# Optimization experiments

Hardware: AMD Instinct MI355X
Metric: run time of the kernel (lower is better)

## Reference

```python
import jax, jax.numpy as jnp
import numpy as np

NUM_HEADS = 16


def setup_inputs() -> dict:
    key = jax.random.key(0)
    k1, k2, k3, k4 = jax.random.split(key, 4)
    B, S, D = 4, 2048, 1024
    x = jax.random.normal(k1, (B, S, D), dtype=jnp.float32)
    mask = jnp.ones((B, S, S), dtype=jnp.int32)
    wq = jax.random.normal(k2, (D, D), dtype=jnp.float32) * (D ** -0.5)
    wk = jax.random.normal(k3, (D, D), dtype=jnp.float32) * (D ** -0.5)
    wv = jax.random.normal(k4, (D, D), dtype=jnp.float32) * (D ** -0.5)
    return {"x": x, "mask": mask, "wq": wq, "wk": wk, "wv": wv}


def reference(x, mask, wq, wk, wv):
    B, S, D = x.shape
    H = NUM_HEADS
    d_k = D // H
    # torch Linear (no bias): y = x @ W.T ; split heads -> [B,H,S,d_k]
    q = (x @ wq.T).reshape(B, S, H, d_k).transpose(0, 2, 1, 3)
    k = (x @ wk.T).reshape(B, S, H, d_k).transpose(0, 2, 1, 3)
    v = (x @ wv.T).reshape(B, S, H, d_k).transpose(0, 2, 1, 3)
    scale = 1.0 / np.sqrt(d_k).astype(np.float32)
    scores = jnp.einsum("bhqd,bhkd->bhqk", q, k) * scale  # [B,H,S,S]
    # masked_fill(mask==0, -1e9); mask broadcast over heads; NO softmax
    scores = jnp.where(mask[:, None, :, :] == 0, jnp.float32(-1e9), scores)
    # dropout is identity in eval mode
    attn = jnp.einsum("bhqk,bhkd->bhqd", scores, v)  # [B,H,S,d_k]
    return attn.transpose(0, 2, 1, 3).reshape(B, S, D)
```

## Files before the change

kernel.cpp:

```cpp
#include <hip/hip_runtime.h>


using u16 = unsigned short;
typedef __attribute__((ext_vector_type(8))) short  short8;
typedef __attribute__((ext_vector_type(4))) short  s16x4;
typedef __attribute__((ext_vector_type(4))) float  f32x4;
typedef __attribute__((ext_vector_type(4))) unsigned short u16x4;
typedef __attribute__((ext_vector_type(4))) int    i32x4;

#define DEV static __device__ __forceinline__

DEV u16 f2b(float f) {
  unsigned u = __float_as_uint(f);
  return (u16)((u + 0x7FFFu + ((u >> 16) & 1u)) >> 16);
}

DEV int swz(int row, int col) { return (row << 6) + (col ^ ((row & 7) << 3)); }

template <typename T>
DEV void gload_lds16(const T* g, T* l) {
  __builtin_amdgcn_global_load_lds((const __attribute__((address_space(1))) unsigned int*)g,
                                   (__attribute__((address_space(3))) unsigned int*)l, 16, 0, 0);
}

__global__ __launch_bounds__(256) void k_convert(const float* __restrict__ x,
                                                 const float* __restrict__ wq,
                                                 const float* __restrict__ wk,
                                                 const float* __restrict__ wv,
                                                 u16* __restrict__ xb, u16* __restrict__ wb) {
  const int NX4 = 2097152;
  const int NW4 = 262144;
  const int total = NX4 + 3 * NW4;
  for (int i = blockIdx.x * blockDim.x + threadIdx.x; i < total; i += gridDim.x * blockDim.x) {
    const float4* src; u16* dst; int j;
    if (i < NX4) { src = (const float4*)x; dst = xb; j = i; }
    else {
      int tw = i - NX4; int wsel = tw >> 18; j = tw & (NW4 - 1);
      src = (const float4*)(wsel == 0 ? wq : (wsel == 1 ? wk : wv));
      dst = wb + (size_t)wsel * 1048576;
    }
    float4 v = src[j];
    u16x4 o; o[0] = f2b(v.x); o[1] = f2b(v.y); o[2] = f2b(v.z); o[3] = f2b(v.w);
    *(u16x4*)(dst + (size_t)j * 4) = o;
  }
}

__global__ __launch_bounds__(256) void k_flags(const int* __restrict__ mask, int* __restrict__ flags) {
  const int bx = blockIdx.x;
  const int b_ = bx >> 9, rem = bx & 511, qt = rem >> 5, kt = rem & 31;
  const int t = threadIdx.x;
  const size_t base = ((size_t)(b_ * 2048 + qt * 128)) * 2048 + kt * 64;
  int az = 0;
#pragma unroll
  for (int kk = 0; kk < 8; ++kk) {
    int i = t + kk * 256;
    int row = i >> 4, c4 = i & 15;
    i32x4 v = *(const i32x4*)(mask + base + (size_t)row * 2048 + c4 * 4);
    az |= (v.x == 0) | (v.y == 0) | (v.z == 0) | (v.w == 0);
  }
  __shared__ int red[4];
  unsigned long long bal = __ballot(az != 0);
  if ((t & 63) == 0) red[t >> 6] = (bal != 0ull);
  __syncthreads();
  if (t == 0) flags[bx] = red[0] | red[1] | red[2] | red[3];
}

__global__ __launch_bounds__(256, 2) void k_proj(const u16* __restrict__ xb, const u16* __restrict__ wb,
                                                 u16* __restrict__ qb, u16* __restrict__ kb,
                                                 u16* __restrict__ vtb) {
  __shared__ u16 lA[128 * 64];
  __shared__ u16 lB[128 * 64];
  const int t = threadIdx.x, wid = t >> 6, lid = t & 63, ln = lid & 15, hi = lid >> 4;
  const int mt = blockIdx.x >> 3, nt = blockIdx.x & 7, which = blockIdx.y;
  const u16* wsrc = wb + (size_t)which * (1024 * 1024);
  const int wm = wid >> 1, wn = wid & 1;

  f32x4 acc[4][4];
#pragma unroll
  for (int a = 0; a < 4; ++a)
#pragma unroll
    for (int b2 = 0; b2 < 4; ++b2) acc[a][b2] = (f32x4){0.f, 0.f, 0.f, 0.f};

  for (int kt = 0; kt < 16; ++kt) {
    __syncthreads();
#pragma unroll
    for (int i = 0; i < 4; ++i) {
      int e = (i * 256 + t) * 8, row = e >> 6;
      int c = (e & 63) ^ ((row & 7) << 3);
      gload_lds16(xb + (size_t)(mt * 128 + row) * 1024 + kt * 64 + c, &lA[i * 2048 + wid * 512]);
      gload_lds16(wsrc + (size_t)(nt * 128 + row) * 1024 + kt * 64 + c, &lB[i * 2048 + wid * 512]);
    }
    __syncthreads();
#pragma unroll
    for (int ks = 0; ks < 2; ++ks) {
      short8 af[4], bfr[4];
#pragma unroll
      for (int mi = 0; mi < 4; ++mi) af[mi] = *(const short8*)&lA[swz(wm * 64 + mi * 16 + ln, ks * 32 + hi * 8)];
#pragma unroll
      for (int ni = 0; ni < 4; ++ni) bfr[ni] = *(const short8*)&lB[swz(wn * 64 + ni * 16 + ln, ks * 32 + hi * 8)];
#pragma unroll
      for (int mi = 0; mi < 4; ++mi)
#pragma unroll
        for (int ni = 0; ni < 4; ++ni)
          acc[mi][ni] = __builtin_amdgcn_mfma_f32_16x16x32_bf16(af[mi], bfr[ni], acc[mi][ni], 0, 0, 0);
    }
  }

  const int m0 = mt * 128 + wm * 64, n0 = nt * 128 + wn * 64;
  if (which == 2) {
#pragma unroll
    for (int mi = 0; mi < 4; ++mi)
#pragma unroll
      for (int ni = 0; ni < 4; ++ni) {
        int mm = m0 + mi * 16 + hi * 4;
        int nn = n0 + ni * 16 + ln;
        int bb = mm >> 11, s0 = mm & 2047, hh = nn >> 6, dd = nn & 63;
        u16x4 pk;
#pragma unroll
        for (int r = 0; r < 4; ++r) pk[r] = f2b(acc[mi][ni][r]);
        *(u16x4*)(vtb + ((size_t)((bb * 16 + hh) * 64 + dd)) * 2048 + s0) = pk;
      }
  } else {
    u16* dst = (which == 1) ? kb : qb;
#pragma unroll
    for (int mi = 0; mi < 4; ++mi)
#pragma unroll
      for (int ni = 0; ni < 4; ++ni) {
        int nn = n0 + ni * 16 + ln;
        int hh = nn >> 6, dd = nn & 63;
#pragma unroll
        for (int r = 0; r < 4; ++r) {
          int m = m0 + mi * 16 + hi * 4 + r;
          int bb = m >> 11, ss = m & 2047;
          dst[((size_t)(bb * 16 + hh) * 2048 + ss) * 64 + dd] = f2b(acc[mi][ni][r]);
        }
      }
  }
}

__global__ __launch_bounds__(256, 2) void k_attn(const u16* __restrict__ qb, const u16* __restrict__ kb,
                                                 const u16* __restrict__ vtb, const int* __restrict__ mask,
                                                 const int* __restrict__ flags, float* __restrict__ out) {
  __shared__ __align__(16) u16 lds[24576];
  const int t = threadIdx.x, wid = t >> 6, lid = t & 63, ln = lid & 15, hi = lid >> 4;
  const int qt = blockIdx.x, bh = blockIdx.y, b_ = bh >> 4, h = bh & 15;
  const u16* Qg = qb + (size_t)bh * (2048 * 64);
  const u16* Kg = kb + (size_t)bh * (2048 * 64);
  const u16* Vg = vtb + (size_t)bh * (64 * 2048);
  const int* flagp = flags + (b_ * 16 + qt) * 32;
  const int* maskp = mask + (size_t)b_ * (2048 * 2048);
  u16* lQ = lds + 16384;

#pragma unroll
  for (int i = 0; i < 4; ++i) {
    int e = (i * 256 + t) * 8, row = e >> 6;
    int c = (e & 63) ^ ((row & 7) << 3);
    gload_lds16(Qg + (size_t)(qt * 128 + row) * 64 + c, &lQ[i * 2048 + wid * 512]);
  }
#pragma unroll
  for (int i = 0; i < 2; ++i) {
    int e = (i * 256 + t) * 8, row = e >> 6;
    int c = (e & 63) ^ ((row & 7) << 3);
    gload_lds16(Kg + (size_t)row * 64 + c, &lds[i * 2048 + wid * 512]);
    gload_lds16(Vg + (size_t)row * 2048 + c, &lds[4096 + i * 2048 + wid * 512]);
  }
  __syncthreads();

  short8 aq[2][2];
#pragma unroll
  for (int mi = 0; mi < 2; ++mi)
#pragma unroll
    for (int ks = 0; ks < 2; ++ks)
      aq[mi][ks] = *(const short8*)&lQ[swz(wid * 32 + mi * 16 + ln, ks * 32 + hi * 8)];

  f32x4 ot[4][2];
#pragma unroll
  for (int di = 0; di < 4; ++di)
#pragma unroll
    for (int mi = 0; mi < 2; ++mi) ot[di][mi] = (f32x4){0.f, 0.f, 0.f, 0.f};

  int cur = 0;
  for (int kt = 0; kt < 32; ++kt) {
    if (kt + 1 < 32) {
#pragma unroll
      for (int i = 0; i < 2; ++i) {
        int e = (i * 256 + t) * 8, row = e >> 6;
        int c = (e & 63) ^ ((row & 7) << 3);
        gload_lds16(Kg + (size_t)((kt + 1) * 64 + row) * 64 + c, &lds[(cur ^ 1) * 8192 + i * 2048 + wid * 512]);
        gload_lds16(Vg + (size_t)row * 2048 + (kt + 1) * 64 + c, &lds[(cur ^ 1) * 8192 + 4096 + i * 2048 + wid * 512]);
      }
    }
    const u16* bK = lds + cur * 8192;
    const u16* bV = lds + cur * 8192 + 4096;

    f32x4 sa[4][2];
#pragma unroll
    for (int ni = 0; ni < 4; ++ni)
#pragma unroll
      for (int mi = 0; mi < 2; ++mi) sa[ni][mi] = (f32x4){0.f, 0.f, 0.f, 0.f};
#pragma unroll
    for (int ks = 0; ks < 2; ++ks) {
      short8 bk[4];
#pragma unroll
      for (int ni = 0; ni < 4; ++ni) bk[ni] = *(const short8*)&bK[swz(ni * 16 + ln, ks * 32 + hi * 8)];
#pragma unroll
      for (int ni = 0; ni < 4; ++ni)
#pragma unroll
        for (int mi = 0; mi < 2; ++mi)
          sa[ni][mi] = __builtin_amdgcn_mfma_f32_16x16x32_bf16(bk[ni], aq[mi][ks], sa[ni][mi], 0, 0, 0);
    }

    int flg = flagp[kt];
    s16x4 pt[4][2];
#pragma unroll
    for (int ni = 0; ni < 4; ++ni)
#pragma unroll
      for (int mi = 0; mi < 2; ++mi) {
#pragma unroll
        for (int r = 0; r < 4; ++r) {
          float p = sa[ni][mi][r] * 0.125f;
          if (flg) {
            int qg = qt * 128 + wid * 32 + mi * 16 + ln;
            int kvg = kt * 64 + ni * 16 + hi * 4 + r;
            if (maskp[(size_t)qg * 2048 + kvg] == 0) p = -1e9f;
          }
          pt[ni][mi][r] = (short)f2b(p);
        }
      }

#pragma unroll
    for (int di = 0; di < 4; ++di) {
      s16x4 vt[4];
#pragma unroll
      for (int ni = 0; ni < 4; ++ni) vt[ni] = *(const s16x4*)&bV[swz(di * 16 + ln, ni * 16 + hi * 4)];
#pragma unroll
      for (int ni = 0; ni < 4; ++ni)
#pragma unroll
        for (int mi = 0; mi < 2; ++mi)
          ot[di][mi] = __builtin_amdgcn_mfma_f32_16x16x16bf16_1k(vt[ni], pt[ni][mi], ot[di][mi], 0, 0, 0);
    }

    __syncthreads();
    cur ^= 1;
  }

  float* op = out + ((size_t)b_ * 2048 + qt * 128) * 1024 + h * 64;
#pragma unroll
  for (int di = 0; di < 4; ++di)
#pragma unroll
    for (int mi = 0; mi < 2; ++mi) {
      int q = wid * 32 + mi * 16 + ln;
      int d = di * 16 + hi * 4;
      *(f32x4*)(op + (size_t)q * 1024 + d) = ot[di][mi];
    }
}

extern "C" void kernel_launch(void* const* d_in, const int* in_sizes, int n_in,
                              void* d_out, int out_size, void* d_ws, size_t ws_size,
                              hipStream_t stream) {
  const float* x   = (const float*)d_in[0];
  const int*  mask = (const int*)d_in[1];
  const float* wq  = (const float*)d_in[2];
  const float* wk  = (const float*)d_in[3];
  const float* wv  = (const float*)d_in[4];
  float* out = (float*)d_out;

  char* ws = (char*)d_ws;
  const size_t XB_OFF = 0;
  const size_t WB_OFF = 16777216;
  const size_t QB_OFF = 23068672;
  const size_t KB_OFF = 39845888;
  const size_t VT_OFF = 56623104;
  const size_t FL_OFF = 73400320;
  if (ws_size < FL_OFF + 8192) return;

  u16* xb  = (u16*)(ws + XB_OFF);
  u16* wb  = (u16*)(ws + WB_OFF);
  u16* qb  = (u16*)(ws + QB_OFF);
  u16* kb  = (u16*)(ws + KB_OFF);
  u16* vtb = (u16*)(ws + VT_OFF);
  int* flags = (int*)(ws + FL_OFF);

  k_convert<<<2048, 256, 0, stream>>>(x, wq, wk, wv, xb, wb);
  k_flags<<<2048, 256, 0, stream>>>(mask, flags);
  k_proj<<<dim3(512, 3), 256, 0, stream>>>(xb, wb, qb, kb, vtb);
  k_attn<<<dim3(16, 64), 256, 0, stream>>>(qb, kb, vtb, mask, flags, out);
}
```

Measured before the change: 321.0 us.

## Merge prep kernels, fold Q scaling into projection, raise attention occupancy

Merges the bf16 conversion and mask-flag kernels into one launch, which removes one launch and lets both memory-bound jobs run together. Folds the 1/sqrt(d_k) scale into the Q projection epilogue so the attention loop skips a multiply per score. Loads Q fragments directly from global memory into registers instead of staging them through LDS, which shrinks LDS use enough to raise the attention launch bound to 4 blocks per CU. It also swaps the hand-written bf16 rounding for the HIP intrinsic. Rounding the pre-scaled Q to bf16 differs slightly from scaling afterwards, and the tighter launch bound may force register spills.

```diff
diff --git a/kernel.cpp b/kernel.cpp
--- a/kernel.cpp
+++ b/kernel.cpp
@@ -1,4 +1,5 @@
 #include <hip/hip_runtime.h>
+#include <hip/hip_bf16.h>
 
 
 using u16 = unsigned short;
@@ -10,9 +11,9 @@
 
 #define DEV static __device__ __forceinline__
 
-DEV u16 f2b(float f) {
-  unsigned u = __float_as_uint(f);
-  return (u16)((u + 0x7FFFu + ((u >> 16) & 1u)) >> 16);
+DEV u16 f2bh(float f) {
+  __hip_bfloat16 h = __float2bfloat16(f);
+  u16 r; __builtin_memcpy(&r, &h, 2); return r;
 }
 
 DEV int swz(int row, int col) { return (row << 6) + (col ^ ((row & 7) << 3)); }
@@ -23,46 +24,48 @@
                                    (__attribute__((address_space(3))) unsigned int*)l, 16, 0, 0);
 }
 
-__global__ __launch_bounds__(256) void k_convert(const float* __restrict__ x,
-                                                 const float* __restrict__ wq,
-                                                 const float* __restrict__ wk,
-                                                 const float* __restrict__ wv,
-                                                 u16* __restrict__ xb, u16* __restrict__ wb) {
-  const int NX4 = 2097152;
-  const int NW4 = 262144;
-  const int total = NX4 + 3 * NW4;
-  for (int i = blockIdx.x * blockDim.x + threadIdx.x; i < total; i += gridDim.x * blockDim.x) {
-    const float4* src; u16* dst; int j;
-    if (i < NX4) { src = (const float4*)x; dst = xb; j = i; }
-    else {
-      int tw = i - NX4; int wsel = tw >> 18; j = tw & (NW4 - 1);
-      src = (const float4*)(wsel == 0 ? wq : (wsel == 1 ? wk : wv));
-      dst = wb + (size_t)wsel * 1048576;
-    }
-    float4 v = src[j];
-    u16x4 o; o[0] = f2b(v.x); o[1] = f2b(v.y); o[2] = f2b(v.z); o[3] = f2b(v.w);
-    *(u16x4*)(dst + (size_t)j * 4) = o;
-  }
-}
-
-__global__ __launch_bounds__(256) void k_flags(const int* __restrict__ mask, int* __restrict__ flags) {
-  const int bx = blockIdx.x;
-  const int b_ = bx >> 9, rem = bx & 511, qt = rem >> 5, kt = rem & 31;
+__global__ __launch_bounds__(256) void k_prep(const float* __restrict__ x,
+                                              const float* __restrict__ wq,
+                                              const float* __restrict__ wk,
+                                              const float* __restrict__ wv,
+                                              const int* __restrict__ mask,
+                                              u16* __restrict__ xb, u16* __restrict__ wb,
+                                              int* __restrict__ flags) {
   const int t = threadIdx.x;
-  const size_t base = ((size_t)(b_ * 2048 + qt * 128)) * 2048 + kt * 64;
-  int az = 0;
-#pragma unroll
-  for (int kk = 0; kk < 8; ++kk) {
-    int i = t + kk * 256;
-    int row = i >> 4, c4 = i & 15;
-    i32x4 v = *(const i32x4*)(mask + base + (size_t)row * 2048 + c4 * 4);
-    az |= (v.x == 0) | (v.y == 0) | (v.z == 0) | (v.w == 0);
-  }
-  __shared__ int red[4];
-  unsigned long long bal = __ballot(az != 0);
-  if ((t & 63) == 0) red[t >> 6] = (bal != 0ull);
-  __syncthreads();
-  if (t == 0) flags[bx] = red[0] | red[1] | red[2] | red[3];
+  if (blockIdx.x < 2048) {
+    const int NX4 = 2097152;
+    const int NW4 = 262144;
+    const int total = NX4 + 3 * NW4;
+    for (int i = blockIdx.x * 256 + t; i < total; i += 2048 * 256) {
+      const float4* src; u16* dst; int j;
+      if (i < NX4) { src = (const float4*)x; dst = xb; j = i; }
+      else {
+        int tw = i - NX4; int wsel = tw >> 18; j = tw & (NW4 - 1);
+        src = (const float4*)(wsel == 0 ? wq : (wsel == 1 ? wk : wv));
+        dst = wb + (size_t)wsel * 1048576;
+      }
+      float4 v = src[j];
+      u16x4 o; o[0] = f2bh(v.x); o[1] = f2bh(v.y); o[2] = f2bh(v.z); o[3] = f2bh(v.w);
+      *(u16x4*)(dst + (size_t)j * 4) = o;
+    }
+  } else {
+    const int bx = blockIdx.x - 2048;
+    const int b_ = bx >> 9, rem = bx & 511, qt = rem >> 5, kt = rem & 31;
+    const size_t base = ((size_t)(b_ * 2048 + qt * 128)) * 2048 + kt * 64;
+    int az = 0;
+#pragma unroll
+    for (int kk = 0; kk < 8; ++kk) {
+      int i = t + kk * 256;
+      int row = i >> 4, c4 = i & 15;
+      i32x4 v = *(const i32x4*)(mask + base + (size_t)row * 2048 + c4 * 4);
+      az |= (v.x == 0) | (v.y == 0) | (v.z == 0) | (v.w == 0);
+    }
+    __shared__ int red[4];
+    unsigned long long bal = __ballot(az != 0);
+    if ((t & 63) == 0) red[t >> 6] = (bal != 0ull);
+    __syncthreads();
+    if (t == 0) flags[bx] = red[0] | red[1] | red[2] | red[3];
+  }
 }
 
 __global__ __launch_bounds__(256, 2) void k_proj(const u16* __restrict__ xb, const u16* __restrict__ wb,
@@ -117,11 +120,12 @@
         int bb = mm >> 11, s0 = mm & 2047, hh = nn >> 6, dd = nn & 63;
         u16x4 pk;
 #pragma unroll
-        for (int r = 0; r < 4; ++r) pk[r] = f2b(acc[mi][ni][r]);
+        for (int r = 0; r < 4; ++r) pk[r] = f2bh(acc[mi][ni][r]);
         *(u16x4*)(vtb + ((size_t)((bb * 16 + hh) * 64 + dd)) * 2048 + s0) = pk;
       }
   } else {
     u16* dst = (which == 1) ? kb : qb;
+    const float sc = (which == 0) ? 0.125f : 1.0f;
 #pragma unroll
     for (int mi = 0; mi < 4; ++mi)
 #pragma unroll
@@ -132,16 +136,16 @@
         for (int r = 0; r < 4; ++r) {
           int m = m0 + mi * 16 + hi * 4 + r;
           int bb = m >> 11, ss = m & 2047;
-          dst[((size_t)(bb * 16 + hh) * 2048 + ss) * 64 + dd] = f2b(acc[mi][ni][r]);
+          dst[((size_t)(bb * 16 + hh) * 2048 + ss) * 64 + dd] = f2bh(acc[mi][ni][r] * sc);
         }
       }
   }
 }
 
-__global__ __launch_bounds__(256, 2) void k_attn(const u16* __restrict__ qb, const u16* __restrict__ kb,
+__global__ __launch_bounds__(256, 4) void k_attn(const u16* __restrict__ qb, const u16* __restrict__ kb,
                                                  const u16* __restrict__ vtb, const int* __restrict__ mask,
                                                  const int* __restrict__ flags, float* __restrict__ out) {
-  __shared__ __align__(16) u16 lds[24576];
+  __shared__ __align__(16) u16 lds[16384];
   const int t = threadIdx.x, wid = t >> 6, lid = t & 63, ln = lid & 15, hi = lid >> 4;
   const int qt = blockIdx.x, bh = blockIdx.y, b_ = bh >> 4, h = bh & 15;
   const u16* Qg = qb + (size_t)bh * (2048 * 64);
@@ -149,14 +153,14 @@
   const u16* Vg = vtb + (size_t)bh * (64 * 2048);
   const int* flagp = flags + (b_ * 16 + qt) * 32;
   const int* maskp = mask + (size_t)b_ * (2048 * 2048);
-  u16* lQ = lds + 16384;
-
-#pragma unroll
-  for (int i = 0; i < 4; ++i) {
-    int e = (i * 256 + t) * 8, row = e >> 6;
-    int c = (e & 63) ^ ((row & 7) << 3);
-    gload_lds16(Qg + (size_t)(qt * 128 + row) * 64 + c, &lQ[i * 2048 + wid * 512]);
-  }
+
+  short8 aq[2][2];
+#pragma unroll
+  for (int mi = 0; mi < 2; ++mi)
+#pragma unroll
+    for (int ks = 0; ks < 2; ++ks)
+      aq[mi][ks] = *(const short8*)(Qg + (size_t)(qt * 128 + wid * 32 + mi * 16 + ln) * 64 + ks * 32 + hi * 8);
+
 #pragma unroll
   for (int i = 0; i < 2; ++i) {
     int e = (i * 256 + t) * 8, row = e >> 6;
@@ -166,13 +170,6 @@
   }
   __syncthreads();
 
-  short8 aq[2][2];
-#pragma unroll
-  for (int mi = 0; mi < 2; ++mi)
-#pragma unroll
-    for (int ks = 0; ks < 2; ++ks)
-      aq[mi][ks] = *(const short8*)&lQ[swz(wid * 32 + mi * 16 + ln, ks * 32 + hi * 8)];
-
   f32x4 ot[4][2];
 #pragma unroll
   for (int di = 0; di < 4; ++di)
@@ -218,13 +215,13 @@
       for (int mi = 0; mi < 2; ++mi) {
 #pragma unroll
         for (int r = 0; r < 4; ++r) {
-          float p = sa[ni][mi][r] * 0.125f;
+          float p = sa[ni][mi][r];
           if (flg) {
             int qg = qt * 128 + wid * 32 + mi * 16 + ln;
             int kvg = kt * 64 + ni * 16 + hi * 4 + r;
             if (maskp[(size_t)qg * 2048 + kvg] == 0) p = -1e9f;
           }
-          pt[ni][mi][r] = (short)f2b(p);
+          pt[ni][mi][r] = (short)f2bh(p);
         }
       }
 
@@ -281,8 +278,7 @@
   u16* vtb = (u16*)(ws + VT_OFF);
   int* flags = (int*)(ws + FL_OFF);
 
-  k_convert<<<2048, 256, 0, stream>>>(x, wq, wk, wv, xb, wb);
-  k_flags<<<2048, 256, 0, stream>>>(mask, flags);
+  k_prep<<<4096, 256, 0, stream>>>(x, wq, wk, wv, mask, xb, wb, flags);
   k_proj<<<dim3(512, 3), 256, 0, stream>>>(xb, wb, qb, kb, vtb);
   k_attn<<<dim3(16, 64), 256, 0, stream>>>(qb, kb, vtb, mask, flags, out);
 }
```

Measured after the change: 298.8 us. -6.9%, faster.
